# Performance work log

Measured on AMD Instinct MI355X. Metric: run time of the kernel, lower is better.

## Reference

```python
import jax, jax.numpy as jnp
import numpy as np

D = 4        # memory depth
K = 64       # number of locations
N = 262144   # number of time units
KAPPA = K + K * K * D


def setup_inputs() -> dict:
    key = jax.random.key(0)
    k_obs, k_beta = jax.random.split(key)
    obs = jax.random.uniform(k_obs, (N, K), dtype=jnp.float32)          # observations (dense stand-in for csr)
    beta = jax.random.uniform(k_beta, (1, KAPPA), dtype=jnp.float32)    # matches uniform_(0, 1) init
    return {"obs": obs, "beta": beta, "d": D}


def reference(obs, beta, d):
    n, k = obs.shape
    beta0 = beta[0, :k]                       # [K] base intensity
    B3 = beta[0, k:].reshape(k, k, d)         # [K, K, d]; B3[k,j,i] multiplies obs[t-d+i, j]
    # sliding windows W[t, i, j] = obs[t + i, j], t = 0..n-d-1  (window ending just before t+d)
    idx = jnp.arange(n - d)[:, None] + jnp.arange(d)[None, :]  # [T', d]
    W = obs[idx]                                               # [T', d, K]
    # lam[t, k] = beta0[k] + sum_{i,j} W[t,i,j] * B3[k,j,i]  (the kron(I_K, vec) matmul collapsed)
    lam = beta0[None, :] + jnp.einsum('tij,kji->tk', W, B3)    # [T', K]
    tgt = obs[d:]                                              # omega_t for t = d..n-1
    loglik = jnp.sum(tgt * jnp.log(lam)) - jnp.sum(lam)
    return loglik, lam
```

## Files before the change

kernel.cpp:

```cpp
#include <hip/hip_runtime.h>
#include <hip/hip_bf16.h>

#define NROWS 262144
#define KO 64
#define DW 4
#define TROWS (NROWS - DW)

using f32x4  = __attribute__((ext_vector_type(4))) float;
using bf16x8 = __attribute__((ext_vector_type(8))) __bf16;

__global__ void pack_b_kernel(const float* __restrict__ beta, __bf16* __restrict__ bpack,
                              float* __restrict__ out0) {
  int idx = blockIdx.x * 256 + threadIdx.x;
  if (idx == 0) out0[0] = 0.f;
  if (idx >= 2048) return;
  int lane = idx & 63;
  int kt = (idx >> 6) & 3;
  int cc = idx >> 8;
  int kout = kt * 16 + (lane & 15);
  int cbase = cc * 32 + 8 * (lane >> 4);
  __bf16* dst = bpack + idx * 8;
#pragma unroll
  for (int e = 0; e < 8; ++e) {
    int c = cbase + e;
    int i = c >> 6;
    int j = c & 63;
    dst[e] = (__bf16)beta[KO + (kout * KO + j) * DW + i];
  }
}

__launch_bounds__(256, 6)
__global__ void poisson_main_kernel(const float* __restrict__ obs,
                                    const float* __restrict__ beta,
                                    const __bf16* __restrict__ bpack,
                                    float* __restrict__ lam_out,
                                    float* __restrict__ loglik) {
  const int wave = threadIdx.x >> 6;
  const int lane = threadIdx.x & 63;
  const int lr = lane & 15;
  const int lg = lane >> 4;
  const int t0 = blockIdx.x * 128 + wave * 32;

  const float* pA[2];
#pragma unroll
  for (int ts = 0; ts < 2; ++ts) {
    int rb = t0 + 16 * ts + lr;
    if (rb > NROWS - 4) rb = NROWS - 4;
    pA[ts] = obs + rb * KO + 8 * lg;
  }

  bf16x8 tgtv[4];
#pragma unroll
  for (int ts = 0; ts < 2; ++ts)
#pragma unroll
    for (int r = 0; r < 4; ++r) {
      int tr = t0 + 16 * ts + 4 * lg + r + DW;
      if (tr > NROWS - 1) tr = NROWS - 1;
      const float* q = obs + tr * KO + lr;
#pragma unroll
      for (int kt = 0; kt < 4; ++kt) {
        const int idx = ts * 16 + r * 4 + kt;
        tgtv[idx >> 3][idx & 7] = (__bf16)q[kt * 16];
      }
    }

  float b0v[4];
#pragma unroll
  for (int kt = 0; kt < 4; ++kt) b0v[kt] = beta[kt * 16 + lr];

  const __bf16* pB = bpack + lane * 8;

  f32x4 acc[2][4];
#pragma unroll
  for (int ts = 0; ts < 2; ++ts)
#pragma unroll
    for (int kt = 0; kt < 4; ++kt)
      acc[ts][kt] = (f32x4){0.f, 0.f, 0.f, 0.f};

#pragma unroll
  for (int cc = 0; cc < 8; ++cc) {
    bf16x8 af[2];
#pragma unroll
    for (int ts = 0; ts < 2; ++ts) {
      const float* p = pA[ts] + (cc >> 1) * KO + (cc & 1) * 32;
      f32x4 f0 = *reinterpret_cast<const f32x4*>(p);
      f32x4 f1 = *reinterpret_cast<const f32x4*>(p + 4);
      bf16x8 av;
      av[0] = (__bf16)f0[0]; av[1] = (__bf16)f0[1];
      av[2] = (__bf16)f0[2]; av[3] = (__bf16)f0[3];
      av[4] = (__bf16)f1[0]; av[5] = (__bf16)f1[1];
      av[6] = (__bf16)f1[2]; av[7] = (__bf16)f1[3];
      af[ts] = av;
    }
#pragma unroll
    for (int kt = 0; kt < 4; ++kt) {
      bf16x8 bfrag = *reinterpret_cast<const bf16x8*>(pB + (cc * 4 + kt) * 512);
      acc[0][kt] = __builtin_amdgcn_mfma_f32_16x16x32_bf16(af[0], bfrag, acc[0][kt], 0, 0, 0);
      acc[1][kt] = __builtin_amdgcn_mfma_f32_16x16x32_bf16(af[1], bfrag, acc[1][kt], 0, 0, 0);
    }
  }

  float part = 0.f;
#pragma unroll
  for (int ts = 0; ts < 2; ++ts)
#pragma unroll
    for (int r = 0; r < 4; ++r) {
      const int t = t0 + 16 * ts + 4 * lg + r;
      if (t < TROWS) {
        float* po = lam_out + t * KO + lr;
#pragma unroll
        for (int kt = 0; kt < 4; ++kt) {
          const float lam = acc[ts][kt][r] + b0v[kt];
          po[kt * 16] = lam;
          const int idx = ts * 16 + r * 4 + kt;
          part += (float)tgtv[idx >> 3][idx & 7] * __logf(lam) - lam;
        }
      }
    }

#pragma unroll
  for (int off = 32; off > 0; off >>= 1)
    part += __shfl_down(part, off, 64);

  __shared__ float wpart[4];
  if (lane == 0) wpart[wave] = part;
  __syncthreads();
  if (threadIdx.x == 0)
    atomicAdd(loglik, wpart[0] + wpart[1] + wpart[2] + wpart[3]);
}

extern "C" void kernel_launch(void* const* d_in, const int* in_sizes, int n_in,
                              void* d_out, int out_size, void* d_ws, size_t ws_size,
                              hipStream_t stream) {
  const float* obs  = (const float*)d_in[0];
  const float* beta = (const float*)d_in[1];
  float* out = (float*)d_out;

  __bf16* bpack = (__bf16*)d_ws;

  hipLaunchKernelGGL(pack_b_kernel, dim3(8), dim3(256), 0, stream, beta, bpack, out);
  hipLaunchKernelGGL(poisson_main_kernel, dim3(2048), dim3(256), 0, stream,
                     obs, beta, bpack, out + 1, out);
}
```

Baseline: 165.6 us.

## Double-buffer obs loads across MFMA groups and defer target loads to epilogue

Restructures the MFMA loop into four groups and prefetches the next group's fp32 observation vectors into a register double buffer while the current group is converted and multiplied. Target-row loads and the base-intensity loads move from the prologue to the epilogue, and targets are now read in fp32 directly rather than stored as bf16. The launch-bounds occupancy hint drops from 6 to 3 blocks to leave room for the larger register footprint. The aim is to hide global-load latency behind MFMA work, at the cost of fewer resident waves and of target loads now sitting on the epilogue's critical path.

```diff
diff --git a/kernel.cpp b/kernel.cpp
--- a/kernel.cpp
+++ b/kernel.cpp
@@ -29,7 +29,7 @@
   }
 }
 
-__launch_bounds__(256, 6)
+__launch_bounds__(256, 3)
 __global__ void poisson_main_kernel(const float* __restrict__ obs,
                                     const float* __restrict__ beta,
                                     const __bf16* __restrict__ bpack,
@@ -48,26 +48,6 @@
     if (rb > NROWS - 4) rb = NROWS - 4;
     pA[ts] = obs + rb * KO + 8 * lg;
   }
-
-  bf16x8 tgtv[4];
-#pragma unroll
-  for (int ts = 0; ts < 2; ++ts)
-#pragma unroll
-    for (int r = 0; r < 4; ++r) {
-      int tr = t0 + 16 * ts + 4 * lg + r + DW;
-      if (tr > NROWS - 1) tr = NROWS - 1;
-      const float* q = obs + tr * KO + lr;
-#pragma unroll
-      for (int kt = 0; kt < 4; ++kt) {
-        const int idx = ts * 16 + r * 4 + kt;
-        tgtv[idx >> 3][idx & 7] = (__bf16)q[kt * 16];
-      }
-    }
-
-  float b0v[4];
-#pragma unroll
-  for (int kt = 0; kt < 4; ++kt) b0v[kt] = beta[kt * 16 + lr];
-
   const __bf16* pB = bpack + lane * 8;
 
   f32x4 acc[2][4];
@@ -77,28 +57,50 @@
     for (int kt = 0; kt < 4; ++kt)
       acc[ts][kt] = (f32x4){0.f, 0.f, 0.f, 0.f};
 
+  f32x4 rbuf[2][8];
+#define LOADG(BUF, G) do {                                                  \
+    _Pragma("unroll")                                                       \
+    for (int ccp = 0; ccp < 2; ++ccp)                                       \
+      _Pragma("unroll")                                                     \
+      for (int ts = 0; ts < 2; ++ts) {                                      \
+        const float* p = pA[ts] + (G) * KO + ccp * 32;                      \
+        rbuf[BUF][ccp * 4 + ts * 2 + 0] = *reinterpret_cast<const f32x4*>(p);     \
+        rbuf[BUF][ccp * 4 + ts * 2 + 1] = *reinterpret_cast<const f32x4*>(p + 4); \
+      }                                                                     \
+  } while (0)
+
+  LOADG(0, 0);
 #pragma unroll
-  for (int cc = 0; cc < 8; ++cc) {
-    bf16x8 af[2];
+  for (int g = 0; g < 4; ++g) {
+    if (g < 3) LOADG((g + 1) & 1, g + 1);
 #pragma unroll
-    for (int ts = 0; ts < 2; ++ts) {
-      const float* p = pA[ts] + (cc >> 1) * KO + (cc & 1) * 32;
-      f32x4 f0 = *reinterpret_cast<const f32x4*>(p);
-      f32x4 f1 = *reinterpret_cast<const f32x4*>(p + 4);
-      bf16x8 av;
-      av[0] = (__bf16)f0[0]; av[1] = (__bf16)f0[1];
-      av[2] = (__bf16)f0[2]; av[3] = (__bf16)f0[3];
-      av[4] = (__bf16)f1[0]; av[5] = (__bf16)f1[1];
-      av[6] = (__bf16)f1[2]; av[7] = (__bf16)f1[3];
-      af[ts] = av;
-    }
+    for (int ccp = 0; ccp < 2; ++ccp) {
+      const int cc = 2 * g + ccp;
+      bf16x8 ax[2];
 #pragma unroll
-    for (int kt = 0; kt < 4; ++kt) {
-      bf16x8 bfrag = *reinterpret_cast<const bf16x8*>(pB + (cc * 4 + kt) * 512);
-      acc[0][kt] = __builtin_amdgcn_mfma_f32_16x16x32_bf16(af[0], bfrag, acc[0][kt], 0, 0, 0);
-      acc[1][kt] = __builtin_amdgcn_mfma_f32_16x16x32_bf16(af[1], bfrag, acc[1][kt], 0, 0, 0);
+      for (int ts = 0; ts < 2; ++ts) {
+        f32x4 f0 = rbuf[g & 1][ccp * 4 + ts * 2 + 0];
+        f32x4 f1 = rbuf[g & 1][ccp * 4 + ts * 2 + 1];
+        bf16x8 av;
+        av[0] = (__bf16)f0[0]; av[1] = (__bf16)f0[1];
+        av[2] = (__bf16)f0[2]; av[3] = (__bf16)f0[3];
+        av[4] = (__bf16)f1[0]; av[5] = (__bf16)f1[1];
+        av[6] = (__bf16)f1[2]; av[7] = (__bf16)f1[3];
+        ax[ts] = av;
+      }
+#pragma unroll
+      for (int kt = 0; kt < 4; ++kt) {
+        bf16x8 bfrag = *reinterpret_cast<const bf16x8*>(pB + (cc * 4 + kt) * 512);
+        acc[0][kt] = __builtin_amdgcn_mfma_f32_16x16x32_bf16(ax[0], bfrag, acc[0][kt], 0, 0, 0);
+        acc[1][kt] = __builtin_amdgcn_mfma_f32_16x16x32_bf16(ax[1], bfrag, acc[1][kt], 0, 0, 0);
+      }
     }
   }
+#undef LOADG
+
+  float b0v[4];
+#pragma unroll
+  for (int kt = 0; kt < 4; ++kt) b0v[kt] = beta[kt * 16 + lr];
 
   float part = 0.f;
 #pragma unroll
@@ -108,12 +110,12 @@
       const int t = t0 + 16 * ts + 4 * lg + r;
       if (t < TROWS) {
         float* po = lam_out + t * KO + lr;
+        const float* ptg = obs + (t + DW) * KO + lr;
 #pragma unroll
         for (int kt = 0; kt < 4; ++kt) {
           const float lam = acc[ts][kt][r] + b0v[kt];
           po[kt * 16] = lam;
-          const int idx = ts * 16 + r * 4 + kt;
-          part += (float)tgtv[idx >> 3][idx & 7] * __logf(lam) - lam;
+          part += ptg[kt * 16] * __logf(lam) - lam;
         }
       }
     }
```

Result: faster. 158.2 us (-4.5%).
